# Optimization experiments

Measured on AMD Instinct MI355X. Metric: run time of the kernel, lower is better.

## Reference

```python
import jax, jax.numpy as jnp
import numpy as np


def _multinomial_sample(t, gumbel, k):
    # t: [R, S] non-negative weights (R = batch*hidden). Torch's
    # torch.multinomial(t, k) (without replacement) is distributionally
    # equivalent to top-k of log(t) + Gumbel noise (Gumbel top-k trick).
    row_sum = jnp.sum(t, axis=1, keepdims=True)          # [R, 1]
    mask = (row_sum == 0).astype(t.dtype)                # [R, 1]
    t = t + mask                                         # zero rows -> uniform
    scores = jnp.log(t) + gumbel                         # log(0) = -inf: never picked
    _, idx = jax.lax.top_k(scores, k)                    # [R, k] sampled w/o replacement
    vals = jnp.take_along_axis(t, idx, axis=1)           # gather sampled weights
    vals = vals + mask * (-1.0)                          # undo the +1 on masked rows
    return vals.sum(axis=1)                              # [R]


def setup_inputs() -> dict:
    key = jax.random.key(0)
    k1, k2, k3, k4 = jax.random.split(key, 4)
    B, S, H = 8, 4096, 1024
    hidden_states = jax.random.normal(k1, (B, S, H), dtype=jnp.float32)
    u = jax.random.uniform(k2, (B * H, S), dtype=jnp.float32, minval=1e-6, maxval=1.0)
    gumbel = -jnp.log(-jnp.log(u))
    W = jax.random.normal(k3, (H, H), dtype=jnp.float32) * 0.02
    b = jax.random.normal(k4, (H,), dtype=jnp.float32) * 0.02
    return {"hidden_states": hidden_states, "gumbel": gumbel, "W": W, "b": b, "sample": 8}


def reference(hidden_states, gumbel, W, b, sample):
    B, S, H = hidden_states.shape
    rep = jax.nn.relu(hidden_states)                     # [B, S, H]
    t = rep.transpose(0, 2, 1).reshape(-1, S)            # [B*H, S]
    pooled = _multinomial_sample(t, gumbel, sample).reshape(B, H)
    out = pooled @ W.T + b                               # nn.Linear(H, H)
    return jnp.tanh(out)
```

## Files before the change

kernel.cpp:

```cpp
#include <hip/hip_runtime.h>
#include <math.h>

#define BB 8
#define SS 4096
#define HH 1024
#define ROWS (BB * HH)
#define KTOP 8

#define INSERT8(TS, TV, SCV, VALV) do {                                   \
    if ((SCV) > TS[7]) {                                                  \
      TS[7] = (SCV); TV[7] = (VALV);                                      \
      _Pragma("unroll")                                                   \
      for (int _i = 7; _i > 0; --_i) {                                    \
        if (TS[_i] > TS[_i - 1]) {                                        \
          float _t = TS[_i]; TS[_i] = TS[_i - 1]; TS[_i - 1] = _t;        \
          float _v = TV[_i]; TV[_i] = TV[_i - 1]; TV[_i - 1] = _v;        \
        }                                                                 \
      }                                                                   \
    }                                                                     \
  } while (0)

__global__ __launch_bounds__(256) void topk_partial(
    const float* __restrict__ hidden, const float* __restrict__ gumbel,
    float2* __restrict__ pairs, int SC) {
  __shared__ float lds_g[256 * 17];
  __shared__ float lds_h[16 * 256];

  const int tid = threadIdx.x;
  const int sc  = blockIdx.x;
  const int rb  = blockIdx.y;
  const int r   = rb * 256 + tid;
  const int b   = rb >> 2;
  const int h0  = (rb & 3) << 8;
  const int s0  = sc * SC;
  const int lane = tid & 63;

  float ts[KTOP], tv[KTOP];
#pragma unroll
  for (int i = 0; i < KTOP; ++i) { ts[i] = -INFINITY; tv[i] = 0.0f; }

  for (int ss = 0; ss < SC; ss += 16) {
    {
      const int si4 = tid & 3;
      const int rl  = tid >> 2;
#pragma unroll
      for (int p = 0; p < 4; ++p) {
        const int row = p * 64 + rl;
        const float4 g4 = *(const float4*)&gumbel[
            (size_t)(rb * 256 + row) * SS + (s0 + ss) + si4 * 4];
        lds_g[row * 17 + si4 * 4 + 0] = g4.x;
        lds_g[row * 17 + si4 * 4 + 1] = g4.y;
        lds_g[row * 17 + si4 * 4 + 2] = g4.z;
        lds_g[row * 17 + si4 * 4 + 3] = g4.w;
      }
    }
    {
      const int srow = tid >> 6;
#pragma unroll
      for (int p = 0; p < 4; ++p) {
        const int si = p * 4 + srow;
        const float4 h4 = *(const float4*)&hidden[
            ((size_t)b * SS + (s0 + ss + si)) * HH + h0 + lane * 4];
        *(float4*)&lds_h[si * 256 + lane * 4] = h4;
      }
    }
    __syncthreads();
#pragma unroll 4
    for (int si = 0; si < 16; ++si) {
      const float t   = fmaxf(lds_h[si * 256 + tid], 0.0f);
      const float g   = lds_g[tid * 17 + si];
      const float scv = logf(t) + g;
      INSERT8(ts, tv, scv, t);
    }
    __syncthreads();
  }
#pragma unroll
  for (int j = 0; j < KTOP; ++j)
    pairs[(size_t)(sc * KTOP + j) * ROWS + r] = make_float2(ts[j], tv[j]);
}

__global__ __launch_bounds__(256) void topk_merge(
    const float2* __restrict__ pairs, float* __restrict__ pooled, int NS) {
  __shared__ float2 ls[64 * 4 * KTOP];
  const int tid  = threadIdx.x;
  const int rloc = tid >> 2;
  const int q    = tid & 3;
  const int r    = blockIdx.x * 64 + rloc;

  float ts[KTOP], tv[KTOP];
#pragma unroll
  for (int i = 0; i < KTOP; ++i) { ts[i] = -INFINITY; tv[i] = 0.0f; }

  const int per = (NS + 3) >> 2;
  const int c0  = q * per;
  const int c1  = (c0 + per < NS) ? (c0 + per) : NS;
  for (int c = c0; c < c1; ++c) {
#pragma unroll
    for (int j = 0; j < KTOP; ++j) {
      const float2 p = pairs[(size_t)(c * KTOP + j) * ROWS + r];
      INSERT8(ts, tv, p.x, p.y);
    }
  }
#pragma unroll
  for (int j = 0; j < KTOP; ++j)
    ls[(rloc * 4 + q) * KTOP + j] = make_float2(ts[j], tv[j]);
  __syncthreads();
  if (q == 0) {
    for (int qq = 1; qq < 4; ++qq) {
#pragma unroll
      for (int j = 0; j < KTOP; ++j) {
        const float2 p = ls[(rloc * 4 + qq) * KTOP + j];
        INSERT8(ts, tv, p.x, p.y);
      }
    }
    float sum = 0.0f;
#pragma unroll
    for (int j = 0; j < KTOP; ++j) sum += tv[j];
    pooled[r] = sum;
  }
}

__global__ __launch_bounds__(256) void linear_tanh(
    const float* __restrict__ pooled, const float* __restrict__ W,
    const float* __restrict__ bias, float* __restrict__ out) {
  __shared__ float lp[ROWS];
  const int tid = threadIdx.x;
  for (int i = tid; i < ROWS / 4; i += 256)
    ((float4*)lp)[i] = ((const float4*)pooled)[i];
  __syncthreads();

  const int wave = tid >> 6;
  const int lane = tid & 63;
#pragma unroll
  for (int jj = 0; jj < 4; ++jj) {
    const int j = blockIdx.x * 16 + wave * 4 + jj;
    float acc[BB];
#pragma unroll
    for (int bb = 0; bb < BB; ++bb) acc[bb] = 0.0f;
    for (int k = 0; k < HH; k += 64) {
      const float w = W[(size_t)j * HH + k + lane];
#pragma unroll
      for (int bb = 0; bb < BB; ++bb) acc[bb] += w * lp[bb * HH + k + lane];
    }
#pragma unroll
    for (int bb = 0; bb < BB; ++bb) {
      float a = acc[bb];
      for (int off = 32; off > 0; off >>= 1) a += __shfl_down(a, off, 64);
      if (lane == 0) out[(size_t)bb * HH + j] = tanhf(a + bias[j]);
    }
  }
}

extern "C" void kernel_launch(void* const* d_in, const int* in_sizes, int n_in,
                              void* d_out, int out_size, void* d_ws, size_t ws_size,
                              hipStream_t stream) {
  const float* hidden = (const float*)d_in[0];
  const float* gumbel = (const float*)d_in[1];
  const float* W      = (const float*)d_in[2];
  const float* bias   = (const float*)d_in[3];
  float* out          = (float*)d_out;

  int NS = 32;
  while (NS > 1) {
    const size_t need = (size_t)NS * KTOP * ROWS * sizeof(float2)
                        + (size_t)ROWS * sizeof(float);
    if (need <= ws_size) break;
    NS >>= 1;
  }
  float2* pairs = (float2*)d_ws;
  float*  pooled = (float*)((char*)d_ws
                   + (size_t)NS * KTOP * ROWS * sizeof(float2));
  const int SC = SS / NS;

  topk_partial<<<dim3(NS, 32), dim3(256), 0, stream>>>(hidden, gumbel, pairs, SC);
  topk_merge<<<dim3(ROWS / 64), dim3(256), 0, stream>>>(pairs, pooled, NS);
  linear_tanh<<<dim3(HH / 16), dim3(256), 0, stream>>>(pooled, W, bias, out);
}
```

Measured before the change: 357.3 us.

## Load gumbel and hidden directly in top-k partial and widen linear kernel

The partial top-k kernel no longer stages gumbel and hidden tiles through LDS with block barriers. Each thread now reads its own gumbel row with two float4 loads and its hidden column with strided scalar loads per 8-step chunk. The aim is to remove LDS traffic and synchronisation, at the cost of gumbel accesses that are poorly coalesced across the wave. The linear+tanh kernel now assigns one output column per wave with float4 loads and launches four times as many blocks.

```diff
diff --git a/kernel.cpp b/kernel.cpp
--- a/kernel.cpp
+++ b/kernel.cpp
@@ -23,9 +23,6 @@
 __global__ __launch_bounds__(256) void topk_partial(
     const float* __restrict__ hidden, const float* __restrict__ gumbel,
     float2* __restrict__ pairs, int SC) {
-  __shared__ float lds_g[256 * 17];
-  __shared__ float lds_h[16 * 256];
-
   const int tid = threadIdx.x;
   const int sc  = blockIdx.x;
   const int rb  = blockIdx.y;
@@ -33,46 +30,29 @@
   const int b   = rb >> 2;
   const int h0  = (rb & 3) << 8;
   const int s0  = sc * SC;
-  const int lane = tid & 63;
+
+  const float* __restrict__ hcol = hidden + (size_t)b * SS * HH + h0 + tid;
+  const float* __restrict__ grow = gumbel + (size_t)r * SS;
 
   float ts[KTOP], tv[KTOP];
 #pragma unroll
   for (int i = 0; i < KTOP; ++i) { ts[i] = -INFINITY; tv[i] = 0.0f; }
 
-  for (int ss = 0; ss < SC; ss += 16) {
-    {
-      const int si4 = tid & 3;
-      const int rl  = tid >> 2;
+  for (int ss = 0; ss < SC; ss += 8) {
+    const int s = s0 + ss;
+    const float4 g0 = *(const float4*)&grow[s];
+    const float4 g1 = *(const float4*)&grow[s + 4];
+    const float* __restrict__ hp = hcol + (size_t)s * HH;
+    float h[8];
 #pragma unroll
-      for (int p = 0; p < 4; ++p) {
-        const int row = p * 64 + rl;
-        const float4 g4 = *(const float4*)&gumbel[
-            (size_t)(rb * 256 + row) * SS + (s0 + ss) + si4 * 4];
-        lds_g[row * 17 + si4 * 4 + 0] = g4.x;
-        lds_g[row * 17 + si4 * 4 + 1] = g4.y;
-        lds_g[row * 17 + si4 * 4 + 2] = g4.z;
-        lds_g[row * 17 + si4 * 4 + 3] = g4.w;
-      }
-    }
-    {
-      const int srow = tid >> 6;
+    for (int i = 0; i < 8; ++i) h[i] = hp[(size_t)i * HH];
+    const float g[8] = {g0.x, g0.y, g0.z, g0.w, g1.x, g1.y, g1.z, g1.w};
 #pragma unroll
-      for (int p = 0; p < 4; ++p) {
-        const int si = p * 4 + srow;
-        const float4 h4 = *(const float4*)&hidden[
-            ((size_t)b * SS + (s0 + ss + si)) * HH + h0 + lane * 4];
-        *(float4*)&lds_h[si * 256 + lane * 4] = h4;
-      }
-    }
-    __syncthreads();
-#pragma unroll 4
-    for (int si = 0; si < 16; ++si) {
-      const float t   = fmaxf(lds_h[si * 256 + tid], 0.0f);
-      const float g   = lds_g[tid * 17 + si];
-      const float scv = logf(t) + g;
+    for (int i = 0; i < 8; ++i) {
+      const float t   = fmaxf(h[i], 0.0f);
+      const float scv = logf(t) + g[i];
       INSERT8(ts, tv, scv, t);
     }
-    __syncthreads();
   }
 #pragma unroll
   for (int j = 0; j < KTOP; ++j)
@@ -125,29 +105,32 @@
     const float* __restrict__ bias, float* __restrict__ out) {
   __shared__ float lp[ROWS];
   const int tid = threadIdx.x;
-  for (int i = tid; i < ROWS / 4; i += 256)
-    ((float4*)lp)[i] = ((const float4*)pooled)[i];
+#pragma unroll
+  for (int i = 0; i < ROWS / 4 / 256; ++i)
+    ((float4*)lp)[i * 256 + tid] = ((const float4*)pooled)[i * 256 + tid];
   __syncthreads();
 
   const int wave = tid >> 6;
   const int lane = tid & 63;
+  const int j = blockIdx.x * 4 + wave;
+
+  float acc[BB];
 #pragma unroll
-  for (int jj = 0; jj < 4; ++jj) {
-    const int j = blockIdx.x * 16 + wave * 4 + jj;
-    float acc[BB];
+  for (int bb = 0; bb < BB; ++bb) acc[bb] = 0.0f;
 #pragma unroll
-    for (int bb = 0; bb < BB; ++bb) acc[bb] = 0.0f;
-    for (int k = 0; k < HH; k += 64) {
-      const float w = W[(size_t)j * HH + k + lane];
-#pragma unroll
-      for (int bb = 0; bb < BB; ++bb) acc[bb] += w * lp[bb * HH + k + lane];
-    }
+  for (int k0 = 0; k0 < HH; k0 += 256) {
+    const float4 w4 = *(const float4*)&W[(size_t)j * HH + k0 + lane * 4];
 #pragma unroll
     for (int bb = 0; bb < BB; ++bb) {
-      float a = acc[bb];
-      for (int off = 32; off > 0; off >>= 1) a += __shfl_down(a, off, 64);
-      if (lane == 0) out[(size_t)bb * HH + j] = tanhf(a + bias[j]);
+      const float4 p4 = *(const float4*)&lp[bb * HH + k0 + lane * 4];
+      acc[bb] += w4.x * p4.x + w4.y * p4.y + w4.z * p4.z + w4.w * p4.w;
     }
+  }
+#pragma unroll
+  for (int bb = 0; bb < BB; ++bb) {
+    float a = acc[bb];
+    for (int off = 32; off > 0; off >>= 1) a += __shfl_down(a, off, 64);
+    if (lane == 0) out[(size_t)bb * HH + j] = tanhf(a + bias[j]);
   }
 }
 
@@ -174,5 +157,5 @@
 
   topk_partial<<<dim3(NS, 32), dim3(256), 0, stream>>>(hidden, gumbel, pairs, SC);
   topk_merge<<<dim3(ROWS / 64), dim3(256), 0, stream>>>(pairs, pooled, NS);
-  linear_tanh<<<dim3(HH / 16), dim3(256), 0, stream>>>(pooled, W, bias, out);
+  linear_tanh<<<dim3(HH / 4), dim3(256), 0, stream>>>(pooled, W, bias, out);
 }
```

Measured after the change: 339.7 us. 4.9% less time.
